# Performance work log

Measured on AMD Instinct MI355X. Metric: run time of the kernel, lower is better.

Reference implementation:

```python
import jax, jax.numpy as jnp
import numpy as np

B, N, F_IN = 8, 1024, 128
H, F_OUT = 4, 64
NEG_INF = -9e15


def setup_inputs() -> dict:
    key = jax.random.key(0)
    k1, k2, k3, k4 = jax.random.split(key, 4)
    x = jax.random.normal(k1, (B, N, F_IN), dtype=jnp.float32)
    adj = jax.random.randint(k2, (B, N, N), 0, 2, dtype=jnp.int32)
    W = jax.random.normal(k3, (F_IN, H * F_OUT), dtype=jnp.float32) * 0.05
    a = jax.random.normal(k4, (H, 2 * F_OUT), dtype=jnp.float32)
    return {"x": x, "adj": adj, "W": W, "a": a}


def reference(x, adj, W, a):
    # x: [B,N,F_in], adj: [B,N,N], W: [F_in, H*F_out], a: [H, 2*F_out]
    Bs, Ns, _ = x.shape
    Hh = a.shape[0]
    Fo = a.shape[1] // 2
    h = (x @ W).reshape(Bs, Ns, Hh, Fo)            # [B,N,H,F]
    # e_{bnmh} = a . cat(h_i, h_j) = a_src . h_n + a_dst . h_m  (no O(N^2) concat)
    a_src, a_dst = a[:, :Fo], a[:, Fo:]
    e_src = jnp.einsum('bnhf,hf->bnh', h, a_src)    # [B,N,H]
    e_dst = jnp.einsum('bmhf,hf->bmh', h, a_dst)    # [B,N,H]
    e = e_src[:, :, None, :] + e_dst[:, None, :, :]  # [B,N,N,H]
    e = jax.nn.leaky_relu(e, negative_slope=0.2)
    e = jnp.where(adj[..., None] > 0, e, NEG_INF)
    attention = jax.nn.softmax(e, axis=2)           # softmax over neighbors m
    h_prime = jnp.einsum('bnmh,bmhf->bnhf', attention, h)
    return h_prime.mean(axis=2)                     # [B,N,F_out]
```

## Files before the change

### kernel.cpp

```cpp
#include <hip/hip_runtime.h>
#include <math.h>

#define Bsz 8
#define Nsz 1024
#define FIN 128
#define Hh  4
#define FO  64
#define COLS 256
#define TN  16
#define TM  32
#define BN  (Bsz*Nsz)
#define SHIFT 12.0f
#define HSTR 40
#define PSTR 136
#define XSTR 136

typedef __attribute__((ext_vector_type(8))) short short8;
typedef __attribute__((ext_vector_type(4))) float f32x4;

static __device__ inline ushort f2bf(float f) {
    uint u = __float_as_uint(f);
    u += 0x7FFFu + ((u >> 16) & 1u);
    return (ushort)(u >> 16);
}
static __device__ inline float bf2f(ushort h) { return __uint_as_float(((uint)h) << 16); }

__global__ __launch_bounds__(256) void gat_prep(const float* __restrict__ W,
                                                ushort* __restrict__ Wt)
{
    const int g = blockIdx.x * 256 + threadIdx.x;
    const int n = g >> 3, kc = (g & 7) * 16;
    ushort u[16];
    #pragma unroll
    for (int i = 0; i < 16; i++) u[i] = f2bf(W[(kc + i) * COLS + n]);
    int4* dst = (int4*)(Wt + n * FIN + kc);
    dst[0] = ((int4*)u)[0];
    dst[1] = ((int4*)u)[1];
}

__global__ __launch_bounds__(256) void gat_proj(
    const float* __restrict__ x, const ushort* __restrict__ Wt,
    const float* __restrict__ a, ushort* __restrict__ h_gB,
    float* __restrict__ es_g, float* __restrict__ ed_g)
{
    __shared__ ushort xs[16 * XSTR];
    const int j    = threadIdx.x;
    const int w    = j >> 6, lane = j & 63, quad = lane >> 4, n16 = lane & 15;
    const int b    = blockIdx.x >> 6, mt16 = blockIdx.x & 63;
    const long rowbase = (long)b * Nsz + mt16 * 16;

    short8 bfr[4][4];
    #pragma unroll
    for (int kk = 0; kk < 4; kk++)
        #pragma unroll
        for (int c4 = 0; c4 < 4; c4++)
            bfr[kk][c4] = *(const short8*)(Wt + (w*64 + c4*16 + n16) * FIN + kk*32 + quad*8);

    {
        const int r = j >> 4, k0 = (j & 15) * 8;
        const float4* g4 = (const float4*)(x + (rowbase + r) * FIN + k0);
        float4 v0 = g4[0], v1 = g4[1];
        ushort u[8] = { f2bf(v0.x), f2bf(v0.y), f2bf(v0.z), f2bf(v0.w),
                        f2bf(v1.x), f2bf(v1.y), f2bf(v1.z), f2bf(v1.w) };
        *(int4*)(xs + r * XSTR + k0) = *(int4*)u;
    }
    __syncthreads();

    f32x4 acc[4];
    #pragma unroll
    for (int c4 = 0; c4 < 4; c4++)
        #pragma unroll
        for (int r = 0; r < 4; r++) acc[c4][r] = 0.f;

    #pragma unroll
    for (int kk = 0; kk < 4; kk++) {
        short8 af = *(const short8*)(xs + n16 * XSTR + kk*32 + quad*8);
        #pragma unroll
        for (int c4 = 0; c4 < 4; c4++)
            acc[c4] = __builtin_amdgcn_mfma_f32_16x16x32_bf16(af, bfr[kk][c4], acc[c4], 0, 0, 0);
    }

    const int mtile = mt16 >> 1;
    const int kbase = (mt16 & 1) * 16 + quad * 4;
    #pragma unroll
    for (int c4 = 0; c4 < 4; c4++) {
        uint2 pk;
        pk.x = (uint)f2bf(acc[c4][0]) | ((uint)f2bf(acc[c4][1]) << 16);
        pk.y = (uint)f2bf(acc[c4][2]) | ((uint)f2bf(acc[c4][3]) << 16);
        const int c = w*64 + c4*16 + n16;
        *(uint2*)(h_gB + (((long)(b*32 + mtile) * COLS + c) * 32 + kbase)) = pk;
    }

    float aS[4], aD[4];
    #pragma unroll
    for (int c4 = 0; c4 < 4; c4++) {
        aS[c4] = a[w * (2*FO) + c4*16 + n16];
        aD[c4] = a[w * (2*FO) + FO + c4*16 + n16];
    }
    #pragma unroll
    for (int reg = 0; reg < 4; reg++) {
        float ps = 0.f, pd = 0.f;
        #pragma unroll
        for (int c4 = 0; c4 < 4; c4++) {
            ps = fmaf(acc[c4][reg], aS[c4], ps);
            pd = fmaf(acc[c4][reg], aD[c4], pd);
        }
        #pragma unroll
        for (int off = 1; off < 16; off <<= 1) {
            ps += __shfl_xor(ps, off, 64);
            pd += __shfl_xor(pd, off, 64);
        }
        if (n16 == 0) {
            const long row = rowbase + quad*4 + reg;
            es_g[(long)w * BN + row] = ps;
            ed_g[(long)w * BN + row] = pd;
        }
    }
}

__global__ __launch_bounds__(256, 3) void gat_attn(
    const int* __restrict__ adj, const ushort* __restrict__ h_gB,
    const float* __restrict__ es_g, const float* __restrict__ ed_g,
    float* __restrict__ out)
{
    __shared__ ushort hT[2][COLS * HSTR];
    __shared__ ushort pT[2][TN * PSTR];
    __shared__ float  l_lds[TN * Hh];

    const int j    = threadIdx.x;
    const int w    = j >> 6, lane = j & 63, quad = lane >> 4, n16 = lane & 15;
    const int mi   = lane & 31, hh = lane >> 5;
    const int b    = blockIdx.y;
    const int n0   = blockIdx.x * TN;
    const long rowb = (long)b * Nsz + n0;

    float es[4][2];
    #pragma unroll
    for (int r4 = 0; r4 < 4; r4++)
        #pragma unroll
        for (int ii = 0; ii < 2; ii++)
            es[r4][ii] = es_g[(long)(hh*2 + ii) * BN + rowb + w*4 + r4];

    f32x4 acc[4];
    #pragma unroll
    for (int c4 = 0; c4 < 4; c4++)
        #pragma unroll
        for (int r = 0; r < 4; r++) acc[c4][r] = 0.f;

    float l_part[4][2];
    #pragma unroll
    for (int r4 = 0; r4 < 4; r4++) { l_part[r4][0] = 0.f; l_part[r4][1] = 0.f; }

    short8 hreg[4]; int areg[4]; float edreg[2];
    const short8* hb8 = (const short8*)h_gB;

#define PREFETCH(t) {                                                           \
    const short8* g = hb8 + (long)(b*32 + (t)) * 1024;                          \
    hreg[0] = g[j]; hreg[1] = g[j+256]; hreg[2] = g[j+512]; hreg[3] = g[j+768]; \
    const int m0p = (t) * TM;                                                   \
    _Pragma("unroll")                                                           \
    for (int r4 = 0; r4 < 4; r4++)                                              \
        areg[r4] = adj[(rowb + w*4 + r4) * (long)Nsz + m0p + mi];               \
    _Pragma("unroll")                                                           \
    for (int ii = 0; ii < 2; ii++)                                              \
        edreg[ii] = ed_g[(long)(hh*2 + ii) * BN + (long)b * Nsz + m0p + mi]; }

#define STAGE(buf) {                                                            \
    _Pragma("unroll")                                                           \
    for (int i = 0; i < 4; i++) {                                               \
        const int s = j + 256*i;                                                \
        *(short8*)(&hT[buf][(s >> 2) * HSTR + (s & 3) * 8]) = hreg[i]; } }

#define PHASE_S(buf) {                                                          \
    _Pragma("unroll")                                                           \
    for (int r4 = 0; r4 < 4; r4++) {                                            \
        _Pragma("unroll")                                                       \
        for (int ii = 0; ii < 2; ii++) {                                        \
            float s = es[r4][ii] + edreg[ii];                                   \
            s = fmaxf(s, 0.2f * s);                                             \
            float p = (areg[r4] > 0) ? __expf(s - SHIFT) : 0.f;                 \
            ushort pb = f2bf(p);                                                \
            pT[buf][(w*4 + r4) * PSTR + (hh*2 + ii) * TM + mi] = pb;            \
            l_part[r4][ii] += bf2f(pb); } } }

#define PHASE_A(buf) {                                                          \
    short8 af = *(const short8*)(&pT[buf][n16 * PSTR + w * TM + quad * 8]);     \
    _Pragma("unroll")                                                           \
    for (int c4 = 0; c4 < 4; c4++) {                                            \
        short8 bfv = *(const short8*)(&hT[buf][(w*64 + c4*16 + n16) * HSTR + quad * 8]); \
        acc[c4] = __builtin_amdgcn_mfma_f32_16x16x32_bf16(af, bfv, acc[c4], 0, 0, 0); } }

    PREFETCH(0);
    STAGE(0); PHASE_S(0);
    PREFETCH(1);
    __syncthreads();

    for (int t = 0; t < Nsz / TM; t++) {
        const int cur = t & 1;
        if (t < Nsz / TM - 1) {
            STAGE(cur ^ 1);
            PHASE_S(cur ^ 1);
            if (t < Nsz / TM - 2) PREFETCH(t + 2);
        }
        PHASE_A(cur);
        __syncthreads();
    }

    #pragma unroll
    for (int r4 = 0; r4 < 4; r4++)
        #pragma unroll
        for (int ii = 0; ii < 2; ii++) {
            float lp = l_part[r4][ii];
            #pragma unroll
            for (int off = 1; off < 32; off <<= 1) lp += __shfl_xor(lp, off, 64);
            if (mi == 0) l_lds[(w*4 + r4) * Hh + hh*2 + ii] = lp;
        }
    __syncthreads();

    float* o_lds = (float*)&hT[0][0];
    float rinv[4];
    #pragma unroll
    for (int reg = 0; reg < 4; reg++)
        rinv[reg] = 0.25f / l_lds[(quad*4 + reg) * Hh + w];
    #pragma unroll
    for (int c4 = 0; c4 < 4; c4++)
        #pragma unroll
        for (int reg = 0; reg < 4; reg++)
            o_lds[(w * TN + quad*4 + reg) * FO + c4*16 + n16] = acc[c4][reg] * rinv[reg];
    __syncthreads();

    {
        const int f2 = j & 63, rb = j >> 6;
        #pragma unroll
        for (int i = 0; i < 4; i++) {
            const int r = i*4 + rb;
            const float sum = o_lds[(0*TN + r)*FO + f2] + o_lds[(1*TN + r)*FO + f2]
                            + o_lds[(2*TN + r)*FO + f2] + o_lds[(3*TN + r)*FO + f2];
            out[(rowb + r) * FO + f2] = sum;
        }
    }
#undef PREFETCH
#undef STAGE
#undef PHASE_S
#undef PHASE_A
}

extern "C" void kernel_launch(void* const* d_in, const int* in_sizes, int n_in,
                              void* d_out, int out_size, void* d_ws, size_t ws_size,
                              hipStream_t stream) {
    const float* x   = (const float*)d_in[0];
    const int*   adj = (const int*)d_in[1];
    const float* W   = (const float*)d_in[2];
    const float* a   = (const float*)d_in[3];
    float* out = (float*)d_out;

    ushort* Wt   = (ushort*)d_ws;
    ushort* h_gB = Wt + (size_t)COLS * FIN;
    float*  es_g = (float*)(h_gB + (size_t)BN * COLS);
    float*  ed_g = es_g + (size_t)Hh * BN;

    gat_prep<<<dim3(8),            dim3(256), 0, stream>>>(W, Wt);
    gat_proj<<<dim3(Bsz*Nsz/16),   dim3(256), 0, stream>>>(x, Wt, a, h_gB, es_g, ed_g);
    gat_attn<<<dim3(Nsz/TN, Bsz),  dim3(256), 0, stream>>>(adj, h_gB, es_g, ed_g, out);
}
```

Baseline: 114.2 us.

## Split neighbor loop across two wave groups and load B fragments directly from global

The attention kernel now runs 512 threads per block, with two 256-thread groups each covering half of the neighbor tiles. Partial accumulators and softmax denominators are combined through LDS at the end. B operands are read straight from global memory into MFMA-fragment registers, removing the shared-memory staging of h. Exponentials use exp2 on log2e-prescaled scores, and pairs of probabilities are packed with a single bf16 conversion instruction. The change relies on gat_proj writing h in a tile-compatible layout. It adds more LDS for the reduction and higher register pressure.

```diff
diff --git a/kernel.cpp b/kernel.cpp
--- a/kernel.cpp
+++ b/kernel.cpp
@@ -10,10 +10,10 @@
 #define TN  16
 #define TM  32
 #define BN  (Bsz*Nsz)
-#define SHIFT 12.0f
-#define HSTR 40
+#define XSTR 136
 #define PSTR 136
-#define XSTR 136
+#define LOG2E  1.44269504088896340f
+#define CSHIFT 17.3123404906675611f
 
 typedef __attribute__((ext_vector_type(8))) short short8;
 typedef __attribute__((ext_vector_type(4))) float f32x4;
@@ -24,6 +24,15 @@
     return (ushort)(u >> 16);
 }
 static __device__ inline float bf2f(ushort h) { return __uint_as_float(((uint)h) << 16); }
+
+static __device__ inline float fexp2(float x) {
+#if __has_builtin(__builtin_amdgcn_exp2f)
+    return __builtin_amdgcn_exp2f(x);
+#else
+    float r; asm("v_exp_f32 %0, %1" : "=v"(r) : "v"(x));
+    return r;
+#endif
+}
 
 __global__ __launch_bounds__(256) void gat_prep(const float* __restrict__ W,
                                                 ushort* __restrict__ Wt)
@@ -112,34 +121,38 @@
         }
         if (n16 == 0) {
             const long row = rowbase + quad*4 + reg;
-            es_g[(long)w * BN + row] = ps;
-            ed_g[(long)w * BN + row] = pd;
-        }
-    }
-}
-
-__global__ __launch_bounds__(256, 3) void gat_attn(
+            es_g[(long)w * BN + row] = ps * LOG2E;
+            ed_g[(long)w * BN + row] = pd * LOG2E;
+        }
+    }
+}
+
+__global__ __launch_bounds__(512, 4) void gat_attn(
     const int* __restrict__ adj, const ushort* __restrict__ h_gB,
     const float* __restrict__ es_g, const float* __restrict__ ed_g,
     float* __restrict__ out)
 {
-    __shared__ ushort hT[2][COLS * HSTR];
-    __shared__ ushort pT[2][TN * PSTR];
-    __shared__ float  l_lds[TN * Hh];
+    __shared__ ushort pT[2][2][TN * PSTR];
+    __shared__ float  o_lds[2][Hh][TN][FO];
+    __shared__ float  l_lds[2][TN][Hh];
 
     const int j    = threadIdx.x;
-    const int w    = j >> 6, lane = j & 63, quad = lane >> 4, n16 = lane & 15;
-    const int mi   = lane & 31, hh = lane >> 5;
-    const int b    = blockIdx.y;
-    const int n0   = blockIdx.x * TN;
+    const int g    = j >> 8;
+    const int jg   = j & 255;
+    const int w    = jg >> 6;
+    const int lane = jg & 63;
+    const int quad = lane >> 4, n16 = lane & 15;
+    const int head = quad;
+    const int mi   = n16 * 2;
+    const int b    = blockIdx.x;
+    const int n0   = blockIdx.y * TN;
     const long rowb = (long)b * Nsz + n0;
-
-    float es[4][2];
+    const int t0   = g * 16;
+
+    float es4[4];
     #pragma unroll
     for (int r4 = 0; r4 < 4; r4++)
-        #pragma unroll
-        for (int ii = 0; ii < 2; ii++)
-            es[r4][ii] = es_g[(long)(hh*2 + ii) * BN + rowb + w*4 + r4];
+        es4[r4] = es_g[(long)head * BN + rowb + w*4 + r4];
 
     f32x4 acc[4];
     #pragma unroll
@@ -147,100 +160,104 @@
         #pragma unroll
         for (int r = 0; r < 4; r++) acc[c4][r] = 0.f;
 
-    float l_part[4][2];
-    #pragma unroll
-    for (int r4 = 0; r4 < 4; r4++) { l_part[r4][0] = 0.f; l_part[r4][1] = 0.f; }
-
-    short8 hreg[4]; int areg[4]; float edreg[2];
-    const short8* hb8 = (const short8*)h_gB;
-
-#define PREFETCH(t) {                                                           \
-    const short8* g = hb8 + (long)(b*32 + (t)) * 1024;                          \
-    hreg[0] = g[j]; hreg[1] = g[j+256]; hreg[2] = g[j+512]; hreg[3] = g[j+768]; \
-    const int m0p = (t) * TM;                                                   \
+    float l_part[4] = {0.f, 0.f, 0.f, 0.f};
+
+    int2   ar[4];
+    float2 edv;
+    short8 bregA[4], bregB[4];
+
+#define PRE_SE(t) {                                                             \
+    const int m0 = (t) * TM + mi;                                               \
     _Pragma("unroll")                                                           \
     for (int r4 = 0; r4 < 4; r4++)                                              \
-        areg[r4] = adj[(rowb + w*4 + r4) * (long)Nsz + m0p + mi];               \
-    _Pragma("unroll")                                                           \
-    for (int ii = 0; ii < 2; ii++)                                              \
-        edreg[ii] = ed_g[(long)(hh*2 + ii) * BN + (long)b * Nsz + m0p + mi]; }
-
-#define STAGE(buf) {                                                            \
-    _Pragma("unroll")                                                           \
-    for (int i = 0; i < 4; i++) {                                               \
-        const int s = j + 256*i;                                                \
-        *(short8*)(&hT[buf][(s >> 2) * HSTR + (s & 3) * 8]) = hreg[i]; } }
-
-#define PHASE_S(buf) {                                                          \
+        ar[r4] = *(const int2*)(adj + (rowb + w*4 + r4) * (long)Nsz + m0);      \
+    edv = *(const float2*)(ed_g + (long)head * BN + (long)b * Nsz + m0); }
+
+#define PRE_B(t, brg) {                                                         \
+    const ushort* hb = h_gB + (long)(b * 32 + (t)) * (COLS * TM);               \
+    _Pragma("unroll")                                                           \
+    for (int c4 = 0; c4 < 4; c4++)                                              \
+        brg[c4] = *(const short8*)(hb + (w*64 + c4*16 + n16) * TM + quad * 8); }
+
+#define PHASE_S(nb) {                                                           \
     _Pragma("unroll")                                                           \
     for (int r4 = 0; r4 < 4; r4++) {                                            \
-        _Pragma("unroll")                                                       \
-        for (int ii = 0; ii < 2; ii++) {                                        \
-            float s = es[r4][ii] + edreg[ii];                                   \
-            s = fmaxf(s, 0.2f * s);                                             \
-            float p = (areg[r4] > 0) ? __expf(s - SHIFT) : 0.f;                 \
-            ushort pb = f2bf(p);                                                \
-            pT[buf][(w*4 + r4) * PSTR + (hh*2 + ii) * TM + mi] = pb;            \
-            l_part[r4][ii] += bf2f(pb); } } }
-
-#define PHASE_A(buf) {                                                          \
-    short8 af = *(const short8*)(&pT[buf][n16 * PSTR + w * TM + quad * 8]);     \
-    _Pragma("unroll")                                                           \
-    for (int c4 = 0; c4 < 4; c4++) {                                            \
-        short8 bfv = *(const short8*)(&hT[buf][(w*64 + c4*16 + n16) * HSTR + quad * 8]); \
-        acc[c4] = __builtin_amdgcn_mfma_f32_16x16x32_bf16(af, bfv, acc[c4], 0, 0, 0); } }
-
-    PREFETCH(0);
-    STAGE(0); PHASE_S(0);
-    PREFETCH(1);
-    __syncthreads();
-
-    for (int t = 0; t < Nsz / TM; t++) {
-        const int cur = t & 1;
-        if (t < Nsz / TM - 1) {
-            STAGE(cur ^ 1);
-            PHASE_S(cur ^ 1);
-            if (t < Nsz / TM - 2) PREFETCH(t + 2);
-        }
-        PHASE_A(cur);
+        float s0 = es4[r4] + edv.x, s1 = es4[r4] + edv.y;                       \
+        float u0 = fmaxf(s0, 0.2f * s0) - CSHIFT;                               \
+        float u1 = fmaxf(s1, 0.2f * s1) - CSHIFT;                               \
+        float e0 = fexp2(u0), e1 = fexp2(u1);                                   \
+        e0 = (ar[r4].x > 0) ? e0 : 0.f;                                         \
+        e1 = (ar[r4].y > 0) ? e1 : 0.f;                                         \
+        uint pk;                                                                \
+        asm("v_cvt_pk_bf16_f32 %0, %1, %2" : "=v"(pk) : "v"(e0), "v"(e1));      \
+        *(uint*)(&pT[g][nb][(w*4 + r4) * PSTR + head * TM + mi]) = pk;          \
+        l_part[r4] += __uint_as_float(pk << 16)                                 \
+                    + __uint_as_float(pk & 0xFFFF0000u); } }
+
+#define PHASE_A(cb, brg) {                                                      \
+    short8 af = *(const short8*)(&pT[g][cb][n16 * PSTR + w * TM + quad * 8]);   \
+    _Pragma("unroll")                                                           \
+    for (int c4 = 0; c4 < 4; c4++)                                              \
+        acc[c4] = __builtin_amdgcn_mfma_f32_16x16x32_bf16(af, brg[c4], acc[c4], 0, 0, 0); }
+
+    PRE_SE(t0);
+    PRE_B(t0, bregA);
+    PHASE_S(0);
+    PRE_SE(t0 + 1);
+    PRE_B(t0 + 1, bregB);
+    __syncthreads();
+
+    for (int i = 0; i < 16; i += 2) {
+        PHASE_S(1);
+        if (i < 14) PRE_SE(t0 + i + 2);
+        PHASE_A(0, bregA);
+        if (i < 14) PRE_B(t0 + i + 2, bregA);
         __syncthreads();
-    }
-
-    #pragma unroll
-    for (int r4 = 0; r4 < 4; r4++)
-        #pragma unroll
-        for (int ii = 0; ii < 2; ii++) {
-            float lp = l_part[r4][ii];
+        if (i < 14) PHASE_S(0);
+        if (i < 14) PRE_SE(t0 + i + 3);
+        PHASE_A(1, bregB);
+        if (i < 14) PRE_B(t0 + i + 3, bregB);
+        __syncthreads();
+    }
+
+    #pragma unroll
+    for (int r4 = 0; r4 < 4; r4++) {
+        float lp = l_part[r4];
+        #pragma unroll
+        for (int off = 1; off < 16; off <<= 1) lp += __shfl_xor(lp, off, 64);
+        if (n16 == 0) l_lds[g][w*4 + r4][head] = lp;
+    }
+    __syncthreads();
+
+    float rinv[4];
+    #pragma unroll
+    for (int reg = 0; reg < 4; reg++) {
+        const int r = quad*4 + reg;
+        rinv[reg] = 0.25f / (l_lds[0][r][w] + l_lds[1][r][w]);
+    }
+    #pragma unroll
+    for (int c4 = 0; c4 < 4; c4++)
+        #pragma unroll
+        for (int reg = 0; reg < 4; reg++)
+            o_lds[g][w][quad*4 + reg][c4*16 + n16] = acc[c4][reg] * rinv[reg];
+    __syncthreads();
+
+    {
+        const int f2 = j & 63, rb = (j >> 6) & 7;
+        #pragma unroll
+        for (int i2 = 0; i2 < 2; i2++) {
+            const int r = i2 * 8 + rb;
+            float s = 0.f;
             #pragma unroll
-            for (int off = 1; off < 32; off <<= 1) lp += __shfl_xor(lp, off, 64);
-            if (mi == 0) l_lds[(w*4 + r4) * Hh + hh*2 + ii] = lp;
-        }
-    __syncthreads();
-
-    float* o_lds = (float*)&hT[0][0];
-    float rinv[4];
-    #pragma unroll
-    for (int reg = 0; reg < 4; reg++)
-        rinv[reg] = 0.25f / l_lds[(quad*4 + reg) * Hh + w];
-    #pragma unroll
-    for (int c4 = 0; c4 < 4; c4++)
-        #pragma unroll
-        for (int reg = 0; reg < 4; reg++)
-            o_lds[(w * TN + quad*4 + reg) * FO + c4*16 + n16] = acc[c4][reg] * rinv[reg];
-    __syncthreads();
-
-    {
-        const int f2 = j & 63, rb = j >> 6;
-        #pragma unroll
-        for (int i = 0; i < 4; i++) {
-            const int r = i*4 + rb;
-            const float sum = o_lds[(0*TN + r)*FO + f2] + o_lds[(1*TN + r)*FO + f2]
-                            + o_lds[(2*TN + r)*FO + f2] + o_lds[(3*TN + r)*FO + f2];
-            out[(rowb + r) * FO + f2] = sum;
-        }
-    }
-#undef PREFETCH
-#undef STAGE
+            for (int gg = 0; gg < 2; gg++)
+                #pragma unroll
+                for (int ww = 0; ww < 4; ww++)
+                    s += o_lds[gg][ww][r][f2];
+            out[(rowb + r) * FO + f2] = s;
+        }
+    }
+#undef PRE_SE
+#undef PRE_B
 #undef PHASE_S
 #undef PHASE_A
 }
@@ -261,5 +278,5 @@
 
     gat_prep<<<dim3(8),            dim3(256), 0, stream>>>(W, Wt);
     gat_proj<<<dim3(Bsz*Nsz/16),   dim3(256), 0, stream>>>(x, Wt, a, h_gB, es_g, ed_g);
-    gat_attn<<<dim3(Nsz/TN, Bsz),  dim3(256), 0, stream>>>(adj, h_gB, es_g, ed_g, out);
-}
+    gat_attn<<<dim3(Bsz, Nsz/TN),  dim3(512), 0, stream>>>(adj, h_gB, es_g, ed_g, out);
+}
```

Result: no change. 112.2 us (-1.8%).
